# Kernel optimization log

Measured on AMD Instinct MI355X. Metric: run time of the kernel, lower is better.

The kernel has to match this reference:

```python
import jax, jax.numpy as jnp
import numpy as np

B, H, S, DH = 2, 16, 2048, 64


def _decay_matrix(num_heads, seqlen):
    # RetNet per-head decay: gamma_h = 1 - 2^{-5-h}, D[h,n,m] = gamma_h^{n-m} for n>=m else 0
    h = np.arange(num_heads)
    gamma = 1.0 - 2.0 ** (-5.0 - h)  # [H]
    n = np.arange(seqlen)[:, None]
    m = np.arange(seqlen)[None, :]
    diff = (n - m).astype(np.float32)  # [S,S]
    D = np.where(diff >= 0, gamma[:, None, None] ** diff[None, :, :], 0.0)
    D = np.nan_to_num(D, nan=0.0)
    return jnp.asarray(D, dtype=jnp.float32)


def setup_inputs() -> dict:
    key = jax.random.key(0)
    kq, kk, kv = jax.random.split(key, 3)
    Q = jax.random.normal(kq, (B, H, S, DH), dtype=jnp.float32)
    K = jax.random.normal(kk, (B, H, S, DH), dtype=jnp.float32)
    V = jax.random.normal(kv, (B, H, S, DH), dtype=jnp.float32)
    D = _decay_matrix(H, S)  # [H,S,S]
    return {"Q": Q, "K": K, "V": V, "D": D}


def reference(Q, K, V, D):
    # scores = Q @ K^T : [B,H,S,S]
    scores = jnp.einsum("bhqd,bhkd->bhqk", Q, K)
    # retention: elementwise decay mask (no softmax), broadcast D over batch
    MSR = scores * D[None, :, :, :]
    out = jnp.einsum("bhqk,bhkd->bhqd", MSR, V)
    return (out, MSR)
```

## Files before the change

### kernel.cpp

```cpp
#include <hip/hip_runtime.h>
#include <hip/hip_bf16.h>
#include <math.h>

#define S_LEN 2048
#define DHEAD 64
#define NHEADS 16
#define NBATCH 2
#define TM 64
#define TN 64
#define CHUNK 8
#define LDSS 72
#define NTHR 256

typedef __attribute__((ext_vector_type(4))) float f32x4;
typedef __attribute__((ext_vector_type(4))) short s16x4;
typedef __attribute__((ext_vector_type(8))) short s16x8;

static __device__ __forceinline__ short f2bf(float f) {
    union { float f; unsigned u; } x; x.f = f;
    unsigned r = (x.u + 0x7fffu + ((x.u >> 16) & 1u)) >> 16;
    return (short)r;
}

__global__ void zero_out_kernel(float* __restrict__ out) {
    size_t i = (size_t)blockIdx.x * NTHR + threadIdx.x;
    ((f32x4*)out)[i] = (f32x4){0.f, 0.f, 0.f, 0.f};
}

__global__ __launch_bounds__(NTHR, 4)
void retnet_fused(const float* __restrict__ Q, const float* __restrict__ K,
                  const float* __restrict__ V, float* __restrict__ out,
                  float* __restrict__ msr) {
    __shared__ short Qs[TM * LDSS];
    __shared__ short Ks[TN * LDSS];
    __shared__ short Vts[DHEAD * LDSS];
    __shared__ short Ps[TM * LDSS];

    const int t   = blockIdx.x;
    const int ch  = blockIdx.y;
    const int bh  = blockIdx.z;
    const int h   = bh & (NHEADS - 1);
    const int tid = threadIdx.x;
    const int w   = tid >> 6;
    const int l   = tid & 63;
    const int n0  = t * TM;

    const int cbeg   = ch * CHUNK;
    const int cend   = cbeg + CHUNK;
    const int mt_end = (t + 1 < cend) ? (t + 1) : cend;

    const float* Qp = Q + (size_t)bh * S_LEN * DHEAD;
    const float* Kp = K + (size_t)bh * S_LEN * DHEAD;
    const float* Vp = V + (size_t)bh * S_LEN * DHEAD;
    float* outp = out + (size_t)bh * S_LEN * DHEAD;
    float* msrp = msr + (size_t)bh * S_LEN * S_LEN;

    const float gamma = 1.0f - exp2f(-5.0f - (float)h);
    const float log2g = (float)log2((double)gamma);
    const float g2 = gamma * gamma;
    const float g3 = g2 * gamma;

    const int colid = l & 15;
    const int quad  = l >> 4;
    const int arow  = (w << 4) + colid;
    const int k0    = quad << 3;
    const int nrow0 = (w << 4) + (quad << 2);

    if (cbeg < mt_end) {
        #pragma unroll
        for (int p = 0; p < 4; ++p) {
            int idx = p * NTHR + tid;
            int row = idx >> 4;
            int c4  = (idx & 15) << 2;
            f32x4 q = *(const f32x4*)(Qp + (n0 + row) * DHEAD + c4);
            s16x4 qb; qb[0]=f2bf(q[0]); qb[1]=f2bf(q[1]); qb[2]=f2bf(q[2]); qb[3]=f2bf(q[3]);
            *(s16x4*)(&Qs[row * LDSS + c4]) = qb;
        }

        const int srow = tid >> 4;
        const int sc4  = (tid & 15) << 2;

        f32x4 kreg[4], vreg[4];
        {
            const int m0 = cbeg * TN;
            #pragma unroll
            for (int p = 0; p < 4; ++p) {
                kreg[p] = *(const f32x4*)(Kp + (size_t)(m0 + (p << 4) + srow) * DHEAD + sc4);
                vreg[p] = *(const f32x4*)(Vp + (size_t)(m0 + l) * DHEAD + (((p << 2) + w) << 2));
            }
        }

        f32x4 accO[4];
        #pragma unroll
        for (int c = 0; c < 4; ++c) accO[c] = (f32x4){0.f,0.f,0.f,0.f};

        for (int mt = cbeg; mt < mt_end; ++mt) {
            const int m0 = mt * TN;
            __syncthreads();

            #pragma unroll
            for (int p = 0; p < 4; ++p) {
                s16x4 kb; kb[0]=f2bf(kreg[p][0]); kb[1]=f2bf(kreg[p][1]);
                          kb[2]=f2bf(kreg[p][2]); kb[3]=f2bf(kreg[p][3]);
                *(s16x4*)(&Ks[((p << 4) + srow) * LDSS + sc4]) = kb;
            }
            #pragma unroll
            for (int p = 0; p < 4; ++p) {
                int d0 = ((p << 2) + w) << 2;
                Vts[(d0 + 0) * LDSS + l] = f2bf(vreg[p][0]);
                Vts[(d0 + 1) * LDSS + l] = f2bf(vreg[p][1]);
                Vts[(d0 + 2) * LDSS + l] = f2bf(vreg[p][2]);
                Vts[(d0 + 3) * LDSS + l] = f2bf(vreg[p][3]);
            }
            if (mt + 1 < mt_end) {
                const int m0n = m0 + TN;
                #pragma unroll
                for (int p = 0; p < 4; ++p) {
                    kreg[p] = *(const f32x4*)(Kp + (size_t)(m0n + (p << 4) + srow) * DHEAD + sc4);
                    vreg[p] = *(const f32x4*)(Vp + (size_t)(m0n + l) * DHEAD + (((p << 2) + w) << 2));
                }
            }
            __syncthreads();

            f32x4 accS[4];
            #pragma unroll
            for (int c = 0; c < 4; ++c) accS[c] = (f32x4){0.f,0.f,0.f,0.f};
            #pragma unroll
            for (int kc = 0; kc < 2; ++kc) {
                s16x8 a = *(const s16x8*)(&Qs[arow * LDSS + (kc << 5) + k0]);
                #pragma unroll
                for (int c = 0; c < 4; ++c) {
                    s16x8 b = *(const s16x8*)(&Ks[((c << 4) + colid) * LDSS + (kc << 5) + k0]);
                    accS[c] = __builtin_amdgcn_mfma_f32_16x16x32_bf16(a, b, accS[c], 0, 0, 0);
                }
            }

            float dec0[4];
            #pragma unroll
            for (int c = 0; c < 4; ++c) {
                int delta0 = (n0 + nrow0) - (m0 + (c << 4) + colid);
                dec0[c] = exp2f((float)delta0 * log2g);
            }
            const bool diag = (mt == t);

            #pragma unroll
            for (int r = 0; r < 4; ++r) {
                const float gr = (r == 0) ? 1.0f : (r == 1) ? gamma : (r == 2) ? g2 : g3;
                const int nloc = nrow0 + r;
                float* rowp = msrp + (size_t)(n0 + nloc) * S_LEN + (m0 + colid);
                short* prow = &Ps[nloc * LDSS + colid];
                #pragma unroll
                for (int c = 0; c < 4; ++c) {
                    float val = accS[c][r] * (dec0[c] * gr);
                    if (diag) {
                        int delta = (n0 + nloc) - (m0 + (c << 4) + colid);
                        if (delta < 0) val = 0.0f;
                    }
                    __builtin_nontemporal_store(val, rowp + (c << 4));
                    prow[c << 4] = f2bf(val);
                }
            }

            #pragma unroll
            for (int kc = 0; kc < 2; ++kc) {
                s16x8 a = *(const s16x8*)(&Ps[arow * LDSS + (kc << 5) + k0]);
                #pragma unroll
                for (int c = 0; c < 4; ++c) {
                    s16x8 b = *(const s16x8*)(&Vts[((c << 4) + colid) * LDSS + (kc << 5) + k0]);
                    accO[c] = __builtin_amdgcn_mfma_f32_16x16x32_bf16(a, b, accO[c], 0, 0, 0);
                }
            }
        }

        #pragma unroll
        for (int c = 0; c < 4; ++c) {
            int d = (c << 4) + colid;
            #pragma unroll
            for (int r = 0; r < 4; ++r) {
                int nloc = nrow0 + r;
                unsafeAtomicAdd(&outp[(n0 + nloc) * DHEAD + d], accO[c][r]);
            }
        }
    }

    const int zbeg = (cbeg > t + 1) ? cbeg : (t + 1);
    if (zbeg < cend) {
        const int z0 = zbeg << 6;
        const int z1 = cend << 6;
        const f32x4 z4 = (f32x4){0.f,0.f,0.f,0.f};
        #pragma unroll
        for (int rp = 0; rp < 4; ++rp) {
            float* rowp = msrp + (size_t)(n0 + (rp << 4) + (tid >> 4)) * S_LEN;
            for (int cc = z0 + ((tid & 15) << 2); cc < z1; cc += 64) {
                __builtin_nontemporal_store(z4, (f32x4*)(rowp + cc));
            }
        }
    }
}

extern "C" void kernel_launch(void* const* d_in, const int* in_sizes, int n_in,
                              void* d_out, int out_size, void* d_ws, size_t ws_size,
                              hipStream_t stream) {
    const float* Q = (const float*)d_in[0];
    const float* K = (const float*)d_in[1];
    const float* V = (const float*)d_in[2];
    float* out = (float*)d_out;
    float* msr = out + (size_t)NBATCH * NHEADS * S_LEN * DHEAD;

    const int o_elems = NBATCH * NHEADS * S_LEN * DHEAD;
    zero_out_kernel<<<o_elems / 4 / NTHR, NTHR, 0, stream>>>(out);

    dim3 grid(S_LEN / TM, S_LEN / TN / CHUNK, NBATCH * NHEADS);
    retnet_fused<<<grid, NTHR, 0, stream>>>(Q, K, V, out, msr);
}
```

Measured before the change: 779.5 us.

## Drop split-K chunking: one block per query tile, direct output stores

Each block now owns one full query tile and walks every key tile up to the diagonal, instead of splitting the key range into chunks across blocks. The zero-init kernel and the atomic adds on the output go away, replaced by plain stores. Block order is reversed so the longest tiles launch first for better load balance. The cost is fewer blocks (1024 rather than 4096) and a heavily uneven amount of work per block, which can leave the GPU underused near the end.

```diff
diff --git a/kernel.cpp b/kernel.cpp
--- a/kernel.cpp
+++ b/kernel.cpp
@@ -8,7 +8,7 @@
 #define NBATCH 2
 #define TM 64
 #define TN 64
-#define CHUNK 8
+#define NTILES (S_LEN / TM)
 #define LDSS 72
 #define NTHR 256
 
@@ -22,11 +22,6 @@
     return (short)r;
 }
 
-__global__ void zero_out_kernel(float* __restrict__ out) {
-    size_t i = (size_t)blockIdx.x * NTHR + threadIdx.x;
-    ((f32x4*)out)[i] = (f32x4){0.f, 0.f, 0.f, 0.f};
-}
-
 __global__ __launch_bounds__(NTHR, 4)
 void retnet_fused(const float* __restrict__ Q, const float* __restrict__ K,
                   const float* __restrict__ V, float* __restrict__ out,
@@ -36,18 +31,13 @@
     __shared__ short Vts[DHEAD * LDSS];
     __shared__ short Ps[TM * LDSS];
 
-    const int t   = blockIdx.x;
-    const int ch  = blockIdx.y;
-    const int bh  = blockIdx.z;
+    const int t   = (NTILES - 1) - blockIdx.x;
+    const int bh  = blockIdx.y;
     const int h   = bh & (NHEADS - 1);
     const int tid = threadIdx.x;
     const int w   = tid >> 6;
     const int l   = tid & 63;
     const int n0  = t * TM;
-
-    const int cbeg   = ch * CHUNK;
-    const int cend   = cbeg + CHUNK;
-    const int mt_end = (t + 1 < cend) ? (t + 1) : cend;
 
     const float* Qp = Q + (size_t)bh * S_LEN * DHEAD;
     const float* Kp = K + (size_t)bh * S_LEN * DHEAD;
@@ -66,132 +56,125 @@
     const int k0    = quad << 3;
     const int nrow0 = (w << 4) + (quad << 2);
 
-    if (cbeg < mt_end) {
+    #pragma unroll
+    for (int p = 0; p < 4; ++p) {
+        int idx = p * NTHR + tid;
+        int row = idx >> 4;
+        int c4  = (idx & 15) << 2;
+        f32x4 q = *(const f32x4*)(Qp + (n0 + row) * DHEAD + c4);
+        s16x4 qb; qb[0]=f2bf(q[0]); qb[1]=f2bf(q[1]); qb[2]=f2bf(q[2]); qb[3]=f2bf(q[3]);
+        *(s16x4*)(&Qs[row * LDSS + c4]) = qb;
+    }
+
+    const int srow = tid >> 4;
+    const int sc4  = (tid & 15) << 2;
+
+    f32x4 kreg[4], vreg[4];
+    #pragma unroll
+    for (int p = 0; p < 4; ++p) {
+        kreg[p] = *(const f32x4*)(Kp + (size_t)((p << 4) + srow) * DHEAD + sc4);
+        vreg[p] = *(const f32x4*)(Vp + (size_t)l * DHEAD + (((p << 2) + w) << 2));
+    }
+
+    f32x4 accO[4];
+    #pragma unroll
+    for (int c = 0; c < 4; ++c) accO[c] = (f32x4){0.f,0.f,0.f,0.f};
+
+    for (int mt = 0; mt <= t; ++mt) {
+        const int m0 = mt * TN;
+        __syncthreads();
+
         #pragma unroll
         for (int p = 0; p < 4; ++p) {
-            int idx = p * NTHR + tid;
-            int row = idx >> 4;
-            int c4  = (idx & 15) << 2;
-            f32x4 q = *(const f32x4*)(Qp + (n0 + row) * DHEAD + c4);
-            s16x4 qb; qb[0]=f2bf(q[0]); qb[1]=f2bf(q[1]); qb[2]=f2bf(q[2]); qb[3]=f2bf(q[3]);
-            *(s16x4*)(&Qs[row * LDSS + c4]) = qb;
+            s16x4 kb; kb[0]=f2bf(kreg[p][0]); kb[1]=f2bf(kreg[p][1]);
+                      kb[2]=f2bf(kreg[p][2]); kb[3]=f2bf(kreg[p][3]);
+            *(s16x4*)(&Ks[((p << 4) + srow) * LDSS + sc4]) = kb;
         }
-
-        const int srow = tid >> 4;
-        const int sc4  = (tid & 15) << 2;
-
-        f32x4 kreg[4], vreg[4];
-        {
-            const int m0 = cbeg * TN;
+        #pragma unroll
+        for (int p = 0; p < 4; ++p) {
+            int d0 = ((p << 2) + w) << 2;
+            Vts[(d0 + 0) * LDSS + l] = f2bf(vreg[p][0]);
+            Vts[(d0 + 1) * LDSS + l] = f2bf(vreg[p][1]);
+            Vts[(d0 + 2) * LDSS + l] = f2bf(vreg[p][2]);
+            Vts[(d0 + 3) * LDSS + l] = f2bf(vreg[p][3]);
+        }
+        if (mt < t) {
+            const int m0n = m0 + TN;
             #pragma unroll
             for (int p = 0; p < 4; ++p) {
-                kreg[p] = *(const f32x4*)(Kp + (size_t)(m0 + (p << 4) + srow) * DHEAD + sc4);
-                vreg[p] = *(const f32x4*)(Vp + (size_t)(m0 + l) * DHEAD + (((p << 2) + w) << 2));
+                kreg[p] = *(const f32x4*)(Kp + (size_t)(m0n + (p << 4) + srow) * DHEAD + sc4);
+                vreg[p] = *(const f32x4*)(Vp + (size_t)(m0n + l) * DHEAD + (((p << 2) + w) << 2));
+            }
+        }
+        __syncthreads();
+
+        f32x4 accS[4];
+        #pragma unroll
+        for (int c = 0; c < 4; ++c) accS[c] = (f32x4){0.f,0.f,0.f,0.f};
+        #pragma unroll
+        for (int kc = 0; kc < 2; ++kc) {
+            s16x8 a = *(const s16x8*)(&Qs[arow * LDSS + (kc << 5) + k0]);
+            #pragma unroll
+            for (int c = 0; c < 4; ++c) {
+                s16x8 b = *(const s16x8*)(&Ks[((c << 4) + colid) * LDSS + (kc << 5) + k0]);
+                accS[c] = __builtin_amdgcn_mfma_f32_16x16x32_bf16(a, b, accS[c], 0, 0, 0);
             }
         }
 
-        f32x4 accO[4];
+        float dec0[4];
         #pragma unroll
-        for (int c = 0; c < 4; ++c) accO[c] = (f32x4){0.f,0.f,0.f,0.f};
+        for (int c = 0; c < 4; ++c) {
+            int delta0 = (n0 + nrow0) - (m0 + (c << 4) + colid);
+            dec0[c] = exp2f((float)delta0 * log2g);
+        }
+        const bool diag = (mt == t);
 
-        for (int mt = cbeg; mt < mt_end; ++mt) {
-            const int m0 = mt * TN;
-            __syncthreads();
-
-            #pragma unroll
-            for (int p = 0; p < 4; ++p) {
-                s16x4 kb; kb[0]=f2bf(kreg[p][0]); kb[1]=f2bf(kreg[p][1]);
-                          kb[2]=f2bf(kreg[p][2]); kb[3]=f2bf(kreg[p][3]);
-                *(s16x4*)(&Ks[((p << 4) + srow) * LDSS + sc4]) = kb;
-            }
-            #pragma unroll
-            for (int p = 0; p < 4; ++p) {
-                int d0 = ((p << 2) + w) << 2;
-                Vts[(d0 + 0) * LDSS + l] = f2bf(vreg[p][0]);
-                Vts[(d0 + 1) * LDSS + l] = f2bf(vreg[p][1]);
-                Vts[(d0 + 2) * LDSS + l] = f2bf(vreg[p][2]);
-                Vts[(d0 + 3) * LDSS + l] = f2bf(vreg[p][3]);
-            }
-            if (mt + 1 < mt_end) {
-                const int m0n = m0 + TN;
-                #pragma unroll
-                for (int p = 0; p < 4; ++p) {
-                    kreg[p] = *(const f32x4*)(Kp + (size_t)(m0n + (p << 4) + srow) * DHEAD + sc4);
-                    vreg[p] = *(const f32x4*)(Vp + (size_t)(m0n + l) * DHEAD + (((p << 2) + w) << 2));
-                }
-            }
-            __syncthreads();
-
-            f32x4 accS[4];
-            #pragma unroll
-            for (int c = 0; c < 4; ++c) accS[c] = (f32x4){0.f,0.f,0.f,0.f};
-            #pragma unroll
-            for (int kc = 0; kc < 2; ++kc) {
-                s16x8 a = *(const s16x8*)(&Qs[arow * LDSS + (kc << 5) + k0]);
-                #pragma unroll
-                for (int c = 0; c < 4; ++c) {
-                    s16x8 b = *(const s16x8*)(&Ks[((c << 4) + colid) * LDSS + (kc << 5) + k0]);
-                    accS[c] = __builtin_amdgcn_mfma_f32_16x16x32_bf16(a, b, accS[c], 0, 0, 0);
-                }
-            }
-
-            float dec0[4];
+        #pragma unroll
+        for (int r = 0; r < 4; ++r) {
+            const float gr = (r == 0) ? 1.0f : (r == 1) ? gamma : (r == 2) ? g2 : g3;
+            const int nloc = nrow0 + r;
+            float* rowp = msrp + (size_t)(n0 + nloc) * S_LEN + (m0 + colid);
+            short* prow = &Ps[nloc * LDSS + colid];
             #pragma unroll
             for (int c = 0; c < 4; ++c) {
-                int delta0 = (n0 + nrow0) - (m0 + (c << 4) + colid);
-                dec0[c] = exp2f((float)delta0 * log2g);
-            }
-            const bool diag = (mt == t);
-
-            #pragma unroll
-            for (int r = 0; r < 4; ++r) {
-                const float gr = (r == 0) ? 1.0f : (r == 1) ? gamma : (r == 2) ? g2 : g3;
-                const int nloc = nrow0 + r;
-                float* rowp = msrp + (size_t)(n0 + nloc) * S_LEN + (m0 + colid);
-                short* prow = &Ps[nloc * LDSS + colid];
-                #pragma unroll
-                for (int c = 0; c < 4; ++c) {
-                    float val = accS[c][r] * (dec0[c] * gr);
-                    if (diag) {
-                        int delta = (n0 + nloc) - (m0 + (c << 4) + colid);
-                        if (delta < 0) val = 0.0f;
-                    }
-                    __builtin_nontemporal_store(val, rowp + (c << 4));
-                    prow[c << 4] = f2bf(val);
+                float val = accS[c][r] * (dec0[c] * gr);
+                if (diag) {
+                    int delta = (n0 + nloc) - (m0 + (c << 4) + colid);
+                    if (delta < 0) val = 0.0f;
                 }
-            }
-
-            #pragma unroll
-            for (int kc = 0; kc < 2; ++kc) {
-                s16x8 a = *(const s16x8*)(&Ps[arow * LDSS + (kc << 5) + k0]);
-                #pragma unroll
-                for (int c = 0; c < 4; ++c) {
-                    s16x8 b = *(const s16x8*)(&Vts[((c << 4) + colid) * LDSS + (kc << 5) + k0]);
-                    accO[c] = __builtin_amdgcn_mfma_f32_16x16x32_bf16(a, b, accO[c], 0, 0, 0);
-                }
+                __builtin_nontemporal_store(val, rowp + (c << 4));
+                prow[c << 4] = f2bf(val);
             }
         }
 
         #pragma unroll
-        for (int c = 0; c < 4; ++c) {
-            int d = (c << 4) + colid;
+        for (int kc = 0; kc < 2; ++kc) {
+            s16x8 a = *(const s16x8*)(&Ps[arow * LDSS + (kc << 5) + k0]);
             #pragma unroll
-            for (int r = 0; r < 4; ++r) {
-                int nloc = nrow0 + r;
-                unsafeAtomicAdd(&outp[(n0 + nloc) * DHEAD + d], accO[c][r]);
+            for (int c = 0; c < 4; ++c) {
+                s16x8 b = *(const s16x8*)(&Vts[((c << 4) + colid) * LDSS + (kc << 5) + k0]);
+                accO[c] = __builtin_amdgcn_mfma_f32_16x16x32_bf16(a, b, accO[c], 0, 0, 0);
             }
         }
     }
 
-    const int zbeg = (cbeg > t + 1) ? cbeg : (t + 1);
-    if (zbeg < cend) {
-        const int z0 = zbeg << 6;
-        const int z1 = cend << 6;
+    #pragma unroll
+    for (int c = 0; c < 4; ++c) {
+        int d = (c << 4) + colid;
+        #pragma unroll
+        for (int r = 0; r < 4; ++r) {
+            int nloc = nrow0 + r;
+            outp[(n0 + nloc) * DHEAD + d] = accO[c][r];
+        }
+    }
+
+    const int z0 = (t + 1) << 6;
+    if (z0 < S_LEN) {
         const f32x4 z4 = (f32x4){0.f,0.f,0.f,0.f};
         #pragma unroll
         for (int rp = 0; rp < 4; ++rp) {
             float* rowp = msrp + (size_t)(n0 + (rp << 4) + (tid >> 4)) * S_LEN;
-            for (int cc = z0 + ((tid & 15) << 2); cc < z1; cc += 64) {
+            for (int cc = z0 + ((tid & 15) << 2); cc < S_LEN; cc += 64) {
                 __builtin_nontemporal_store(z4, (f32x4*)(rowp + cc));
             }
         }
@@ -207,9 +190,6 @@
     float* out = (float*)d_out;
     float* msr = out + (size_t)NBATCH * NHEADS * S_LEN * DHEAD;
 
-    const int o_elems = NBATCH * NHEADS * S_LEN * DHEAD;
-    zero_out_kernel<<<o_elems / 4 / NTHR, NTHR, 0, stream>>>(out);
-
-    dim3 grid(S_LEN / TM, S_LEN / TN / CHUNK, NBATCH * NHEADS);
+    dim3 grid(NTILES, NBATCH * NHEADS);
     retnet_fused<<<grid, NTHR, 0, stream>>>(Q, K, V, out, msr);
 }
```

After: 772.7 us. About the same (-0.9%).
